# Performance work log

Measured on AMD Instinct MI355X. Metric: run time of the kernel, lower is better.

Reference implementation:

```python
import jax, jax.numpy as jnp
import numpy as np

D_MODEL = 1024
D_INNER = 2048      # expand=2
D_STATE = 128
NHEADS = 32
HEADDIM = 64
DCONV = 4
CONV_DIM = D_INNER + 2 * D_STATE                 # x, B, C channels through conv
D_IN_PROJ = 2 * D_INNER + 2 * D_STATE + NHEADS   # z, xBC, dt
NBLOCKS = 4


def _mlp(x, w1, b1, w2, b2):
    # MLP(2, in, out): Linear(in,in) -> ReLU -> Linear(in,out)
    return jax.nn.relu(x @ w1 + b1) @ w2 + b2


def _mamba2_block(u, Wi, cw, cb, dtb, Alog, Dsk, nw, Wo):
    B, L, _ = u.shape
    zxbcdt = u @ Wi                                        # [B,L,D_IN_PROJ]
    z, xBC, dt = jnp.split(zxbcdt, [D_INNER, D_INNER + CONV_DIM], axis=-1)
    # causal depthwise conv1d, kernel 4
    pad = jnp.pad(xBC, ((0, 0), (DCONV - 1, 0), (0, 0)))
    conv = cb
    for k in range(DCONV):
        conv = conv + pad[:, k:k + L, :] * cw[:, k]
    xBC = jax.nn.silu(conv)
    xh, Bm, Cm = jnp.split(xBC, [D_INNER, D_INNER + D_STATE], axis=-1)
    dt = jax.nn.softplus(dt + dtb)                         # [B,L,H]
    A = -jnp.exp(Alog)                                     # [H], negative
    xh = xh.reshape(B, L, NHEADS, HEADDIM)

    def step(h, inp):
        x_t, dt_t, b_t, c_t = inp                          # [B,H,P],[B,H],[B,N],[B,N]
        dA = jnp.exp(dt_t * A)                             # [B,H]
        h = h * dA[..., None, None] + (dt_t[..., None] * x_t)[..., None] * b_t[:, None, None, :]
        y = jnp.einsum('bhpn,bn->bhp', h, c_t)
        return h, y

    h0 = jnp.zeros((B, NHEADS, HEADDIM, D_STATE), u.dtype)
    _, ys = jax.lax.scan(step, h0, (xh.transpose(1, 0, 2, 3), dt.transpose(1, 0, 2),
                                    Bm.transpose(1, 0, 2), Cm.transpose(1, 0, 2)))
    y = ys.transpose(1, 0, 2, 3) + Dsk[None, None, :, None] * xh   # D skip per head
    y = y.reshape(B, L, D_INNER)
    y = y * jax.nn.silu(z)                                 # gated RMSNorm (gate before norm)
    y = y * jax.lax.rsqrt(jnp.mean(y * y, axis=-1, keepdims=True) + 1e-5) * nw
    return y @ Wo


def setup_inputs() -> dict:
    key = jax.random.key(0)
    ks = jax.random.split(key, 16)
    B, S, STATE = 4, 512, 510
    s = 0.02
    return {
        'x': jax.random.normal(ks[0], (B, S, STATE), jnp.float32),
        'steps_left': jax.random.uniform(ks[1], (B, S, 1), jnp.float32) * 100.0,
        'current_r': jax.random.normal(ks[2], (B, S, 1), jnp.float32),
        'mlp_in_w1': jax.random.normal(ks[3], (STATE + 2, STATE + 2), jnp.float32) * s,
        'mlp_in_b1': jnp.zeros((STATE + 2,), jnp.float32),
        'mlp_in_w2': jax.random.normal(ks[4], (STATE + 2, D_MODEL), jnp.float32) * s,
        'mlp_in_b2': jnp.zeros((D_MODEL,), jnp.float32),
        'W_in': jax.random.normal(ks[5], (NBLOCKS, D_MODEL, D_IN_PROJ), jnp.float32) * s,
        'conv_w': jax.random.normal(ks[6], (NBLOCKS, CONV_DIM, DCONV), jnp.float32) * 0.2,
        'conv_b': jnp.zeros((NBLOCKS, CONV_DIM), jnp.float32),
        'dt_bias': jax.random.normal(ks[7], (NBLOCKS, NHEADS), jnp.float32) * 0.1,
        'A_log': jnp.log(jax.random.uniform(ks[8], (NBLOCKS, NHEADS), jnp.float32, 1.0, 16.0)),
        'D_skip': jnp.ones((NBLOCKS, NHEADS), jnp.float32),
        'norm_w': jnp.ones((NBLOCKS, D_INNER), jnp.float32),
        'W_out': jax.random.normal(ks[9], (NBLOCKS, D_INNER, D_MODEL), jnp.float32) * s,
        'mlp_out_w1': jax.random.normal(ks[10], (D_MODEL, D_MODEL), jnp.float32) * s,
        'mlp_out_b1': jnp.zeros((D_MODEL,), jnp.float32),
        'mlp_out_w2': jax.random.normal(ks[11], (D_MODEL, 1), jnp.float32) * s,
        'mlp_out_b2': jnp.zeros((1,), jnp.float32),
    }


def reference(x, steps_left, current_r,
              mlp_in_w1, mlp_in_b1, mlp_in_w2, mlp_in_b2,
              W_in, conv_w, conv_b, dt_bias, A_log, D_skip, norm_w, W_out,
              mlp_out_w1, mlp_out_b1, mlp_out_w2, mlp_out_b2):
    h = jnp.concatenate([x, steps_left, current_r], axis=-1)   # [B,S,state+2]
    h = _mlp(h, mlp_in_w1, mlp_in_b1, mlp_in_w2, mlp_in_b2)
    for i in range(NBLOCKS):
        h = _mamba2_block(h, W_in[i], conv_w[i], conv_b[i], dt_bias[i],
                          A_log[i], D_skip[i], norm_w[i], W_out[i])
    return _mlp(h, mlp_out_w1, mlp_out_b1, mlp_out_w2, mlp_out_b2)  # [B,S,1]
```

## Files before the change

### kernel.cpp

```cpp
#include <hip/hip_runtime.h>
#include <hip/hip_bf16.h>
#include <math.h>

#define D_MODEL   1024
#define D_INNER   2048
#define D_STATE   128
#define NHEADS    32
#define HEADDIM   64
#define DCONV     4
#define CONV_DIM  (D_INNER + 2 * D_STATE)
#define D_IN_PROJ (2 * D_INNER + 2 * D_STATE + NHEADS)
#define NBLOCKS   4
#define BATCH     4
#define SEQ       512
#define NTOK      (BATCH * SEQ)
#define STATE_IN  510
#define NPAD_IN   4480
#define NSEG      8
#define SEGLEN    64
#define NBH       (BATCH * NHEADS)
#define OFF_B     D_INNER
#define OFF_C     (D_INNER + D_STATE)
#define OFF_DT    (D_IN_PROJ - NHEADS)

typedef _Float16 half8_t __attribute__((ext_vector_type(8)));
typedef float f32x4_t  __attribute__((ext_vector_type(4)));
typedef unsigned short us;

__device__ __forceinline__ us f2h(float f) {
    _Float16 h = (_Float16)f;
    return __builtin_bit_cast(us, h);
}
__device__ __forceinline__ float h2f(us u) {
    return (float)__builtin_bit_cast(_Float16, u);
}
__device__ __forceinline__ void gl2lds16(const us* gp, us* lp) {
    __builtin_amdgcn_global_load_lds(
        (const __attribute__((address_space(1))) unsigned int*)(gp),
        (__attribute__((address_space(3))) unsigned int*)(lp), 16, 0, 0);
}

__global__ void concat_kernel(const float* __restrict__ x,
                              const float* __restrict__ steps,
                              const float* __restrict__ curr,
                              us* __restrict__ hcat)
{
    int idx = blockIdx.x * 256 + threadIdx.x;
    if (idx >= NTOK * 512) return;
    int bl = idx >> 9;
    int c  = idx & 511;
    float v;
    if (c < STATE_IN)       v = x[(size_t)bl * STATE_IN + c];
    else if (c == STATE_IN) v = steps[bl];
    else                    v = curr[bl];
    hcat[idx] = f2h(v);
}

#define NT_TRANS 27904
__global__ __launch_bounds__(256)
void transpose_all_kernel(const float* __restrict__ mi_w1, const float* __restrict__ mi_w2,
                          const float* __restrict__ W_in, const float* __restrict__ W_out,
                          const float* __restrict__ mo_w1,
                          us* __restrict__ wt_mi1, us* __restrict__ wt_mi2,
                          us* __restrict__ wt_in, us* __restrict__ wt_out,
                          us* __restrict__ wt_mo1)
{
    int bid = blockIdx.x;
    const float* W; us* WT; int K, N, ntx, r;
    if (bid < 256)        { W = mi_w1; WT = wt_mi1; K = 512;  N = 512;  ntx = 16;  r = bid; }
    else if (bid < 768)   { W = mi_w2; WT = wt_mi2; K = 512;  N = 1024; ntx = 32;  r = bid - 256; }
    else if (bid < 18688) {
        int rel = bid - 768, i = rel / 4480;
        r = rel - i * 4480;
        W  = W_in  + (size_t)i * D_MODEL * D_IN_PROJ;
        WT = wt_in + (size_t)i * NPAD_IN * 1024;
        K = 1024; N = D_IN_PROJ; ntx = 140;
    }
    else if (bid < 26880) {
        int rel = bid - 18688, i = rel / 2048;
        r = rel - i * 2048;
        W  = W_out  + (size_t)i * D_INNER * D_MODEL;
        WT = wt_out + (size_t)i * 1024 * 2048;
        K = 2048; N = 1024; ntx = 32;
    }
    else { W = mo_w1; WT = wt_mo1; K = 1024; N = 1024; ntx = 32; r = bid - 26880; }
    int n0 = (r % ntx) * 32, k0 = (r / ntx) * 32;

    __shared__ us tile[32][36];
    int t = threadIdx.x;
    int kl = t >> 3, nl = (t & 7) * 4;
    float4 v = make_float4(0.f, 0.f, 0.f, 0.f);
    if (n0 < N) v = *(const float4*)(W + (size_t)(k0 + kl) * N + n0 + nl);
    tile[nl + 0][kl] = f2h(v.x);
    tile[nl + 1][kl] = f2h(v.y);
    tile[nl + 2][kl] = f2h(v.z);
    tile[nl + 3][kl] = f2h(v.w);
    __syncthreads();
    int nl2 = t >> 3, kl2 = (t & 7) * 4;
    ushort4 o;
    o.x = tile[nl2][kl2 + 0];
    o.y = tile[nl2][kl2 + 1];
    o.z = tile[nl2][kl2 + 2];
    o.w = tile[nl2][kl2 + 3];
    *(ushort4*)(WT + (size_t)(n0 + nl2) * K + k0 + kl2) = o;
}

#define PHASE(TT, CUR, STG)                                                     \
    {                                                                           \
        if ((TT) == NT - 1)                                                     \
            asm volatile("s_waitcnt vmcnt(0)" ::: "memory");                    \
        else if constexpr (BN == 128)                                           \
            asm volatile("s_waitcnt vmcnt(4)" ::: "memory");                    \
        else                                                                    \
            asm volatile("s_waitcnt vmcnt(3)" ::: "memory");                    \
        __builtin_amdgcn_s_barrier();                                           \
        if ((TT) + 2 < NT) stage(STG, ((TT) + 2) << 5);                         \
        half8_t af[TI], bfr[4];                                                 \
        _Pragma("unroll")                                                       \
        for (int ti = 0; ti < TI; ++ti) {                                       \
            int rr = wr + ti * 16 + l16;                                        \
            af[ti] = *(const half8_t*)&Al[CUR][rr * 32 + ((g ^ ((rr >> 2) & 3)) * 8)]; \
        }                                                                       \
        _Pragma("unroll")                                                       \
        for (int tj = 0; tj < 4; ++tj) {                                        \
            int rr = wc + tj * 16 + l16;                                        \
            bfr[tj] = *(const half8_t*)&Bl[CUR][rr * 32 + ((g ^ ((rr >> 2) & 3)) * 8)]; \
        }                                                                       \
        _Pragma("unroll")                                                       \
        for (int ti = 0; ti < TI; ++ti)                                         \
            _Pragma("unroll")                                                   \
            for (int tj = 0; tj < 4; ++tj)                                      \
                acc[ti][tj] = __builtin_amdgcn_mfma_f32_16x16x32_f16(           \
                    af[ti], bfr[tj], acc[ti][tj], 0, 0, 0);                     \
    }

template<int BN, int TI>
__global__ __launch_bounds__(256)
void mfma_gemm_f16(const us* __restrict__ A, const us* __restrict__ BT,
                   const float* __restrict__ bias, us* __restrict__ C,
                   int N, int K, int relu)
{
    __shared__ __attribute__((aligned(16))) us Al[3][128 * 32];
    __shared__ __attribute__((aligned(16))) us Bl[3][BN * 32];
    const int tid = threadIdx.x, lane = tid & 63, wave = tid >> 6;
    const int g = lane >> 4, l16 = lane & 15;
    const int wr = (BN == 128) ? (wave >> 1) * 64 : wave * 32;
    const int wc = (BN == 128) ? (wave & 1) * 64 : 0;
    const int m0 = blockIdx.y * 128, n0 = blockIdx.x * BN;
    const int lrow = lane >> 2;
    const int lcol = ((lane & 3) ^ ((lrow >> 2) & 3)) * 8;

    f32x4_t acc[TI][4];
    const f32x4_t zero = {0.f, 0.f, 0.f, 0.f};
#pragma unroll
    for (int i = 0; i < TI; ++i)
#pragma unroll
        for (int j = 0; j < 4; ++j) acc[i][j] = zero;

    const us* abase = A  + (size_t)m0 * K;
    const us* bbase = BT + (size_t)n0 * K;

    auto stage = [&](int buf, int k0) {
#pragma unroll
        for (int s = 0; s < 2; ++s) {
            int rb = wave * 32 + s * 16;
            gl2lds16(abase + (size_t)(rb + lrow) * K + k0 + lcol, &Al[buf][rb * 32]);
        }
#pragma unroll
        for (int s = 0; s < BN / 64; ++s) {
            int rb = wave * (BN / 4) + s * 16;
            gl2lds16(bbase + (size_t)(rb + lrow) * K + k0 + lcol, &Bl[buf][rb * 32]);
        }
    };

    const int NT = K >> 5;
    stage(0, 0);
    stage(1, 32);

    for (int t = 0; t < NT; t += 3) {
        PHASE(t, 0, 2)
        if (t + 1 < NT) PHASE(t + 1, 1, 0)
        if (t + 2 < NT) PHASE(t + 2, 2, 1)
    }

#pragma unroll
    for (int tj = 0; tj < 4; ++tj) {
        int col = n0 + wc + tj * 16 + l16;
        if (col >= N) continue;
        float bv = bias ? bias[col] : 0.f;
#pragma unroll
        for (int ti = 0; ti < TI; ++ti) {
            int rbase = m0 + wr + ti * 16 + g * 4;
#pragma unroll
            for (int r = 0; r < 4; ++r) {
                float v = acc[ti][tj][r] + bv;
                if (relu) v = fmaxf(v, 0.f);
                C[(size_t)(rbase + r) * N + col] = f2h(v);
            }
        }
    }
}

__global__ __launch_bounds__(256)
void conv_silu_kernel(const us* __restrict__ zxbcdt,
                      const float* __restrict__ cw,
                      const float* __restrict__ cb,
                      us* __restrict__ xBCc)
{
    int idx = blockIdx.x * 256 + threadIdx.x;
    if (idx >= NTOK * (CONV_DIM / 4)) return;
    int cq = idx % (CONV_DIM / 4);
    int bl = idx / (CONV_DIM / 4);
    int b  = bl >> 9;
    int l  = bl & 511;
    int c  = cq * 4;
    float4 w0 = *(const float4*)&cw[(c + 0) * DCONV];
    float4 w1 = *(const float4*)&cw[(c + 1) * DCONV];
    float4 w2 = *(const float4*)&cw[(c + 2) * DCONV];
    float4 w3 = *(const float4*)&cw[(c + 3) * DCONV];
    float4 bb = *(const float4*)&cb[c];
    float a0 = bb.x, a1 = bb.y, a2 = bb.z, a3 = bb.w;
    const us* base = zxbcdt + (size_t)(b * SEQ) * D_IN_PROJ + D_INNER + c;
#pragma unroll
    for (int k = 0; k < DCONV; ++k) {
        int ll = l + k - (DCONV - 1);
        if (ll >= 0) {
            ushort4 u = *(const ushort4*)(base + (size_t)ll * D_IN_PROJ);
            a0 = fmaf(h2f(u.x), ((const float*)&w0)[k], a0);
            a1 = fmaf(h2f(u.y), ((const float*)&w1)[k], a1);
            a2 = fmaf(h2f(u.z), ((const float*)&w2)[k], a2);
            a3 = fmaf(h2f(u.w), ((const float*)&w3)[k], a3);
        }
    }
    ushort4 o;
    o.x = f2h(a0 / (1.f + __expf(-a0)));
    o.y = f2h(a1 / (1.f + __expf(-a1)));
    o.z = f2h(a2 / (1.f + __expf(-a2)));
    o.w = f2h(a3 / (1.f + __expf(-a3)));
    *(ushort4*)(xBCc + (size_t)bl * CONV_DIM + c) = o;
}

__global__ __launch_bounds__(256)
void scan_seg_mfma_kernel(const us* __restrict__ zx, const us* __restrict__ xc,
                          const float* __restrict__ dt_bias,
                          const float* __restrict__ A_log,
                          const float* __restrict__ D_skip,
                          float* __restrict__ y, float* __restrict__ alpha,
                          us* __restrict__ Hseg)
{
    __shared__ __attribute__((aligned(16))) us Csh[64 * 128];
    __shared__ __attribute__((aligned(16))) us Bsh[64 * 128];
    __shared__ __attribute__((aligned(16))) us Bt[128 * 64];
    __shared__ __attribute__((aligned(16))) us Xt[64 * 64];
    __shared__ float dt_s[64], ls[64], csc[64];
    us* Ssh = Csh;
    const int bi = blockIdx.x, bh = bi >> 3, seg = bi & 7;
    const int b = bh >> 5, h = bh & 31;
    const int tid = threadIdx.x, lane = tid & 63, w = tid >> 6;
    const int g = lane >> 4, l16 = lane & 15;
    const int t0g = seg * SEGLEN;
    const size_t rowbase = (size_t)(b * SEQ + t0g);

    {
        int rr = lane >> 4, s = lane & 15;
#pragma unroll
        for (int it = 0; it < 4; ++it) {
            int rb = w * 16 + it * 4;
            int row = rb + rr;
            const us* src = xc + (rowbase + row) * CONV_DIM;
            int sw = (s ^ (row & 7)) * 8;
            gl2lds16(src + OFF_C + sw, &Csh[rb * 128]);
            gl2lds16(src + OFF_B + sw, &Bsh[rb * 128]);
        }
    }
#pragma unroll
    for (int qi = 0; qi < 4; ++qi) {
        int idx = tid + qi * 256;
        int pq = idx & 15, j = idx >> 4;
        ushort4 v = *(const ushort4*)(xc + (rowbase + j) * CONV_DIM + h * 64 + pq * 4);
#pragma unroll
        for (int e = 0; e < 4; ++e) {
            int p = pq * 4 + e;
            int pc = ((((j >> 3) ^ (p & 7)) << 3) | (j & 7));
            Xt[p * 64 + pc] = ((const us*)&v)[e];
        }
    }
#pragma unroll
    for (int qi = 0; qi < 8; ++qi) {
        int idx = tid + qi * 256;
        int nq = idx & 31, j = idx >> 5;
        ushort4 v = *(const ushort4*)(xc + (rowbase + j) * CONV_DIM + OFF_B + nq * 4);
#pragma unroll
        for (int e = 0; e < 4; ++e) {
            int n = nq * 4 + e;
            int pc = ((((j >> 3) ^ (n & 7)) << 3) | (j & 7));
            Bt[n * 64 + pc] = ((const us*)&v)[e];
        }
    }
    if (tid < 64) {
        int j = tid;
        float dtraw = h2f(zx[(rowbase + j) * D_IN_PROJ + OFF_DT + h]) + dt_bias[h];
        float dtv = (dtraw > 20.f) ? dtraw : log1pf(expf(dtraw));
        float ld = dtv * (-expf(A_log[h]));
#pragma unroll
        for (int o = 1; o < 64; o <<= 1) {
            float v = __shfl_up(ld, o);
            if (j >= o) ld += v;
        }
        float al = expf(ld);
        dt_s[j] = dtv;
        ls[j] = ld;
        alpha[(size_t)bh * SEQ + t0g + j] = al;
        float cend = __shfl(ld, 63);
        csc[j] = dtv * expf(cend - ld);
    }
    __syncthreads();

    const float Dsk = D_skip[h];
    const f32x4_t vzero = {0.f, 0.f, 0.f, 0.f};

    f32x4_t acc1[4];
#pragma unroll
    for (int jt = 0; jt < 4; ++jt) acc1[jt] = vzero;
    {
        int ia = w * 16 + l16;
#pragma unroll
        for (int ks = 0; ks < 4; ++ks) {
            half8_t a = *(const half8_t*)&Csh[ia * 128 + (((ks * 4 + g) ^ (ia & 7)) << 3)];
#pragma unroll
            for (int jt = 0; jt < 4; ++jt) {
                int jr = jt * 16 + l16;
                half8_t bfr = *(const half8_t*)&Bsh[jr * 128 + (((ks * 4 + g) ^ (jr & 7)) << 3)];
                acc1[jt] = __builtin_amdgcn_mfma_f32_16x16x32_f16(a, bfr, acc1[jt], 0, 0, 0);
            }
        }
    }
    __syncthreads();

    {
        int i0 = w * 16 + g * 4;
        float lsi[4];
#pragma unroll
        for (int r = 0; r < 4; ++r) lsi[r] = ls[i0 + r];
#pragma unroll
        for (int jt = 0; jt < 4; ++jt) {
            int j = jt * 16 + l16;
            float lj = ls[j], dj = dt_s[j];
#pragma unroll
            for (int r = 0; r < 4; ++r) {
                int i = i0 + r;
                float v = 0.f;
                if (j < i)       v = acc1[jt][r] * dj * __expf(lsi[r] - lj);
                else if (j == i) v = acc1[jt][r] * dj + Dsk;
                int pc = ((((j >> 3) ^ (i & 7)) << 3) | (j & 7));
                Ssh[i * 64 + pc] = f2h(v);
            }
        }
    }
    __syncthreads();

    f32x4_t acc2[4];
#pragma unroll
    for (int nt = 0; nt < 4; ++nt) acc2[nt] = vzero;
    {
        int ia = w * 16 + l16;
#pragma unroll
        for (int ks = 0; ks < 2; ++ks) {
            half8_t a = *(const half8_t*)&Ssh[ia * 64 + (((ks * 4 + g) ^ (ia & 7)) << 3)];
#pragma unroll
            for (int nt = 0; nt < 4; ++nt) {
                int pr = nt * 16 + l16;
                half8_t bfr = *(const half8_t*)&Xt[pr * 64 + (((ks * 4 + g) ^ (pr & 7)) << 3)];
                acc2[nt] = __builtin_amdgcn_mfma_f32_16x16x32_f16(a, bfr, acc2[nt], 0, 0, 0);
            }
        }
    }
    {
        int i0 = w * 16 + g * 4;
#pragma unroll
        for (int nt = 0; nt < 4; ++nt) {
            int p = nt * 16 + l16;
#pragma unroll
            for (int r = 0; r < 4; ++r)
                y[(rowbase + i0 + r) * D_INNER + h * 64 + p] = acc2[nt][r];
        }
    }
    f32x4_t acc3[8];
#pragma unroll
    for (int nt = 0; nt < 8; ++nt) acc3[nt] = vzero;
    {
        int pa = w * 16 + l16;
#pragma unroll
        for (int ks = 0; ks < 2; ++ks) {
            half8_t araw = *(const half8_t*)&Xt[pa * 64 + (((ks * 4 + g) ^ (pa & 7)) << 3)];
            half8_t a;
#pragma unroll
            for (int e = 0; e < 8; ++e)
                a[e] = (_Float16)((float)araw[e] * csc[ks * 32 + g * 8 + e]);
#pragma unroll
            for (int nt = 0; nt < 8; ++nt) {
                int nr = nt * 16 + l16;
                half8_t bfr = *(const half8_t*)&Bt[nr * 64 + (((ks * 4 + g) ^ (nr & 7)) << 3)];
                acc3[nt] = __builtin_amdgcn_mfma_f32_16x16x32_f16(a, bfr, acc3[nt], 0, 0, 0);
            }
        }
    }
    {
        int p0 = w * 16 + g * 4;
#pragma unroll
        for (int nt = 0; nt < 8; ++nt) {
            int n = nt * 16 + l16;
#pragma unroll
            for (int r = 0; r < 4; ++r)
                Hseg[((size_t)bi * 64 + p0 + r) * 128 + n] = f2h(acc3[nt][r]);
        }
    }
}

__global__ __launch_bounds__(512)
void state_fixup_kernel(const float* __restrict__ alpha, us* __restrict__ Hseg)
{
    const int bh = blockIdx.x;
    const int t = threadIdx.x, p = t >> 3, ng = t & 7;
    float carry[16];
#pragma unroll
    for (int j = 0; j < 16; ++j) carry[j] = 0.f;
    for (int seg = 0; seg < NSEG; ++seg) {
        us* hs = Hseg + (((size_t)bh * NSEG + seg) * 64 + p) * 128;
        float ae = alpha[(size_t)bh * SEQ + seg * SEGLEN + SEGLEN - 1];
        float tmp[16];
#pragma unroll
        for (int q = 0; q < 4; ++q) {
            ushort4 u = *(const ushort4*)(hs + ng * 4 + q * 32);
            tmp[q*4+0] = h2f(u.x); tmp[q*4+1] = h2f(u.y);
            tmp[q*4+2] = h2f(u.z); tmp[q*4+3] = h2f(u.w);
        }
#pragma unroll
        for (int q = 0; q < 4; ++q) {
            ushort4 o;
            o.x = f2h(carry[q*4+0]); o.y = f2h(carry[q*4+1]);
            o.z = f2h(carry[q*4+2]); o.w = f2h(carry[q*4+3]);
            *(ushort4*)(hs + ng * 4 + q * 32) = o;
        }
#pragma unroll
        for (int j = 0; j < 16; ++j) carry[j] = fmaf(carry[j], ae, tmp[j]);
    }
}

__global__ __launch_bounds__(256)
void correct_mfma_kernel(const us* __restrict__ xc, const float* __restrict__ alpha,
                         const us* __restrict__ Hseg, float* __restrict__ y)
{
    __shared__ __attribute__((aligned(16))) us Csh[64 * 128];
    __shared__ __attribute__((aligned(16))) us Hsh[64 * 128];
    __shared__ float als_s[64];
    const int bi = blockIdx.x;
    const int bh = bi / 7, seg = 1 + (bi % 7);
    const int b = bh >> 5, h = bh & 31;
    const int tid = threadIdx.x, lane = tid & 63, w = tid >> 6;
    const int g = lane >> 4, l16 = lane & 15;
    const int t0g = seg * SEGLEN;
    const size_t rowbase = (size_t)(b * SEQ + t0g);
    const size_t hbase = (size_t)(bh * NSEG + seg) * 64;

    {
        int rr = lane >> 4, s = lane & 15;
#pragma unroll
        for (int it = 0; it < 4; ++it) {
            int rb = w * 16 + it * 4;
            int row = rb + rr;
            int sw = (s ^ (row & 7)) * 8;
            gl2lds16(xc + (rowbase + row) * CONV_DIM + OFF_C + sw, &Csh[rb * 128]);
            gl2lds16(Hseg + (hbase + row) * 128 + sw, &Hsh[rb * 128]);
        }
    }
    if (tid < 64) als_s[tid] = alpha[(size_t)bh * SEQ + t0g + tid];
    __syncthreads();

    const f32x4_t vzero = {0.f, 0.f, 0.f, 0.f};
    f32x4_t acc[4];
#pragma unroll
    for (int nt = 0; nt < 4; ++nt) acc[nt] = vzero;
    int ia = w * 16 + l16;
#pragma unroll
    for (int ks = 0; ks < 4; ++ks) {
        half8_t a = *(const half8_t*)&Csh[ia * 128 + (((ks * 4 + g) ^ (ia & 7)) << 3)];
#pragma unroll
        for (int nt = 0; nt < 4; ++nt) {
            int pr = nt * 16 + l16;
            half8_t bfr = *(const half8_t*)&Hsh[pr * 128 + (((ks * 4 + g) ^ (pr & 7)) << 3)];
            acc[nt] = __builtin_amdgcn_mfma_f32_16x16x32_f16(a, bfr, acc[nt], 0, 0, 0);
        }
    }
    int i0 = w * 16 + g * 4;
#pragma unroll
    for (int nt = 0; nt < 4; ++nt) {
        int p = nt * 16 + l16;
#pragma unroll
        for (int r = 0; r < 4; ++r) {
            size_t idx = (rowbase + i0 + r) * D_INNER + h * 64 + p;
            y[idx] += als_s[i0 + r] * acc[nt][r];
        }
    }
}

__global__ __launch_bounds__(256)
void gated_rmsnorm_kernel(const float* __restrict__ y,
                          const us* __restrict__ zxbcdt,
                          const float* __restrict__ norm_w,
                          us* __restrict__ yn)
{
    int bl = blockIdx.x;
    int t  = threadIdx.x;
    const float* yr = y + (size_t)bl * D_INNER;
    const us* zr = zxbcdt + (size_t)bl * D_IN_PROJ;
    us* outr = yn + (size_t)bl * D_INNER;

    float gv[8];
    float ss = 0.f;
#pragma unroll
    for (int q = 0; q < 8; ++q) {
        int j = t + q * 256;
        float z = h2f(zr[j]);
        float g = yr[j] * (z / (1.f + __expf(-z)));
        gv[q] = g;
        ss += g * g;
    }
    __shared__ float red[256];
    red[t] = ss;
    __syncthreads();
    for (int w = 128; w > 0; w >>= 1) {
        if (t < w) red[t] += red[t + w];
        __syncthreads();
    }
    float rs = rsqrtf(red[0] / (float)D_INNER + 1e-5f);
#pragma unroll
    for (int q = 0; q < 8; ++q) {
        int j = t + q * 256;
        outr[j] = f2h(gv[q] * rs * norm_w[j]);
    }
}

__global__ __launch_bounds__(256)
void final_dot_kernel(const us* __restrict__ t1,
                      const float* __restrict__ w2,
                      const float* __restrict__ b2,
                      float* __restrict__ out)
{
    int bl = blockIdx.x;
    int t  = threadIdx.x;
    float s = 0.f;
    for (int j = t; j < D_MODEL; j += 256)
        s = fmaf(h2f(t1[(size_t)bl * D_MODEL + j]), w2[j], s);
    __shared__ float red[256];
    red[t] = s;
    __syncthreads();
    for (int w = 128; w > 0; w >>= 1) {
        if (t < w) red[t] += red[t + w];
        __syncthreads();
    }
    if (t == 0) out[bl] = red[0] + b2[0];
}

extern "C" void kernel_launch(void* const* d_in, const int* in_sizes, int n_in,
                              void* d_out, int out_size, void* d_ws, size_t ws_size,
                              hipStream_t stream)
{
    const float* x        = (const float*)d_in[0];
    const float* steps    = (const float*)d_in[1];
    const float* curr     = (const float*)d_in[2];
    const float* mi_w1    = (const float*)d_in[3];
    const float* mi_b1    = (const float*)d_in[4];
    const float* mi_w2    = (const float*)d_in[5];
    const float* mi_b2    = (const float*)d_in[6];
    const float* W_in     = (const float*)d_in[7];
    const float* conv_w   = (const float*)d_in[8];
    const float* conv_b   = (const float*)d_in[9];
    const float* dt_bias  = (const float*)d_in[10];
    const float* A_log    = (const float*)d_in[11];
    const float* D_skip   = (const float*)d_in[12];
    const float* norm_w   = (const float*)d_in[13];
    const float* W_out    = (const float*)d_in[14];
    const float* mo_w1    = (const float*)d_in[15];
    const float* mo_b1    = (const float*)d_in[16];
    const float* mo_w2    = (const float*)d_in[17];
    const float* mo_b2    = (const float*)d_in[18];
    float* out = (float*)d_out;

    us* wt_mi1 = (us*)d_ws;
    us* wt_mi2 = wt_mi1 + (size_t)512 * 512;
    us* wt_in  = wt_mi2 + (size_t)1024 * 512;
    us* wt_out = wt_in  + (size_t)4 * NPAD_IN * 1024;
    us* wt_mo1 = wt_out + (size_t)4 * 1024 * 2048;
    us* Hseg   = wt_mo1 + (size_t)1024 * 1024;
    us* hcat   = Hseg   + (size_t)NBH * NSEG * 64 * 128;
    us* h      = hcat   + (size_t)NTOK * 512;
    us* zxb    = h      + (size_t)NTOK * D_MODEL;
    us* xc     = zxb    + (size_t)NTOK * D_IN_PROJ;
    us* yn     = xc     + (size_t)NTOK * CONV_DIM;
    us* t0     = zxb;
    us* t1     = xc;
    float* fbase = (float*)((((uintptr_t)(yn + (size_t)NTOK * D_INNER)) + 255)
                            & ~(uintptr_t)255);
    float* y     = fbase;
    float* alpha = y + (size_t)NTOK * D_INNER;

    transpose_all_kernel<<<NT_TRANS, 256, 0, stream>>>(
        mi_w1, mi_w2, W_in, W_out, mo_w1,
        wt_mi1, wt_mi2, wt_in, wt_out, wt_mo1);

    concat_kernel<<<(NTOK * 512 + 255) / 256, 256, 0, stream>>>(x, steps, curr, hcat);

    mfma_gemm_f16<64, 2><<<dim3(512/64, NTOK/128), 256, 0, stream>>>(
        hcat, wt_mi1, mi_b1, t0, 512, 512, 1);
    mfma_gemm_f16<64, 2><<<dim3(1024/64, NTOK/128), 256, 0, stream>>>(
        t0, wt_mi2, mi_b2, h, 1024, 512, 0);

    for (int i = 0; i < NBLOCKS; ++i) {
        mfma_gemm_f16<128, 4><<<dim3(NPAD_IN/128, NTOK/128), 256, 0, stream>>>(
            h, wt_in + (size_t)i * NPAD_IN * 1024, nullptr, zxb, D_IN_PROJ, D_MODEL, 0);
        conv_silu_kernel<<<(NTOK * (CONV_DIM/4) + 255) / 256, 256, 0, stream>>>(
            zxb, conv_w + (size_t)i * CONV_DIM * DCONV, conv_b + (size_t)i * CONV_DIM, xc);
        scan_seg_mfma_kernel<<<NBH * NSEG, 256, 0, stream>>>(
            zxb, xc, dt_bias + i * NHEADS, A_log + i * NHEADS, D_skip + i * NHEADS,
            y, alpha, Hseg);
        state_fixup_kernel<<<NBH, 512, 0, stream>>>(alpha, Hseg);
        correct_mfma_kernel<<<NBH * (NSEG - 1), 256, 0, stream>>>(xc, alpha, Hseg, y);
        gated_rmsnorm_kernel<<<NTOK, 256, 0, stream>>>(
            y, zxb, norm_w + (size_t)i * D_INNER, yn);
        mfma_gemm_f16<64, 2><<<dim3(1024/64, NTOK/128), 256, 0, stream>>>(
            yn, wt_out + (size_t)i * 1024 * 2048, nullptr, h, 1024, 2048, 0);
    }

    mfma_gemm_f16<64, 2><<<dim3(1024/64, NTOK/128), 256, 0, stream>>>(
        h, wt_mo1, mo_b1, t1, 1024, 1024, 1);
    final_dot_kernel<<<NTOK, 256, 0, stream>>>(t1, mo_w2, mo_b2, out);
}
```

Before: 747.9 us.

## Use larger weight-transpose tiles, smaller MLP-in GEMM tiles, and split state fixup

The weight transpose kernel now handles 64x64 fp32 tiles per block instead of 32x32. It stores fp32 in a padded LDS tile and writes 8-wide fp16 vectors, so far fewer blocks are launched. The GEMM template gains a BM parameter, and the two small input-MLP GEMMs now use 64x64 tiles to put more blocks on the device. The state fixup kernel splits each head's state across two blocks to double its parallelism. The trade-offs are more LDS per transpose block and lower per-block reuse in the small GEMMs.

```diff
diff --git a/kernel.cpp b/kernel.cpp
--- a/kernel.cpp
+++ b/kernel.cpp
@@ -26,6 +26,7 @@
 typedef _Float16 half8_t __attribute__((ext_vector_type(8)));
 typedef float f32x4_t  __attribute__((ext_vector_type(4)));
 typedef unsigned short us;
+typedef unsigned short us8 __attribute__((ext_vector_type(8)));
 
 __device__ __forceinline__ us f2h(float f) {
     _Float16 h = (_Float16)f;
@@ -56,7 +57,7 @@
     hcat[idx] = f2h(v);
 }
 
-#define NT_TRANS 27904
+#define NT_TRANS 6976
 __global__ __launch_bounds__(256)
 void transpose_all_kernel(const float* __restrict__ mi_w1, const float* __restrict__ mi_w2,
                           const float* __restrict__ W_in, const float* __restrict__ W_out,
@@ -67,52 +68,60 @@
 {
     int bid = blockIdx.x;
     const float* W; us* WT; int K, N, ntx, r;
-    if (bid < 256)        { W = mi_w1; WT = wt_mi1; K = 512;  N = 512;  ntx = 16;  r = bid; }
-    else if (bid < 768)   { W = mi_w2; WT = wt_mi2; K = 512;  N = 1024; ntx = 32;  r = bid - 256; }
-    else if (bid < 18688) {
-        int rel = bid - 768, i = rel / 4480;
-        r = rel - i * 4480;
+    if (bid < 64)        { W = mi_w1; WT = wt_mi1; K = 512;  N = 512;  ntx = 8;  r = bid; }
+    else if (bid < 192)  { W = mi_w2; WT = wt_mi2; K = 512;  N = 1024; ntx = 16; r = bid - 64; }
+    else if (bid < 4672) {
+        int rel = bid - 192, i = rel / 1120;
+        r = rel - i * 1120;
         W  = W_in  + (size_t)i * D_MODEL * D_IN_PROJ;
         WT = wt_in + (size_t)i * NPAD_IN * 1024;
-        K = 1024; N = D_IN_PROJ; ntx = 140;
-    }
-    else if (bid < 26880) {
-        int rel = bid - 18688, i = rel / 2048;
-        r = rel - i * 2048;
+        K = 1024; N = D_IN_PROJ; ntx = 70;
+    }
+    else if (bid < 6720) {
+        int rel = bid - 4672, i = rel / 512;
+        r = rel - i * 512;
         W  = W_out  + (size_t)i * D_INNER * D_MODEL;
         WT = wt_out + (size_t)i * 1024 * 2048;
-        K = 2048; N = 1024; ntx = 32;
-    }
-    else { W = mo_w1; WT = wt_mo1; K = 1024; N = 1024; ntx = 32; r = bid - 26880; }
-    int n0 = (r % ntx) * 32, k0 = (r / ntx) * 32;
-
-    __shared__ us tile[32][36];
+        K = 2048; N = 1024; ntx = 16;
+    }
+    else { W = mo_w1; WT = wt_mo1; K = 1024; N = 1024; ntx = 16; r = bid - 6720; }
+    int n0 = (r % ntx) * 64, k0 = (r / ntx) * 64;
+
+    __shared__ float tile[64][65];
     int t = threadIdx.x;
-    int kl = t >> 3, nl = (t & 7) * 4;
-    float4 v = make_float4(0.f, 0.f, 0.f, 0.f);
-    if (n0 < N) v = *(const float4*)(W + (size_t)(k0 + kl) * N + n0 + nl);
-    tile[nl + 0][kl] = f2h(v.x);
-    tile[nl + 1][kl] = f2h(v.y);
-    tile[nl + 2][kl] = f2h(v.z);
-    tile[nl + 3][kl] = f2h(v.w);
+    int kl = t >> 4;
+    int nl = (t & 15) * 4;
+#pragma unroll
+    for (int it = 0; it < 4; ++it) {
+        int k = kl + it * 16;
+        float4 v = make_float4(0.f, 0.f, 0.f, 0.f);
+        if (n0 + nl < N) v = *(const float4*)(W + (size_t)(k0 + k) * N + n0 + nl);
+        tile[k][nl + 0] = v.x; tile[k][nl + 1] = v.y;
+        tile[k][nl + 2] = v.z; tile[k][nl + 3] = v.w;
+    }
     __syncthreads();
-    int nl2 = t >> 3, kl2 = (t & 7) * 4;
-    ushort4 o;
-    o.x = tile[nl2][kl2 + 0];
-    o.y = tile[nl2][kl2 + 1];
-    o.z = tile[nl2][kl2 + 2];
-    o.w = tile[nl2][kl2 + 3];
-    *(ushort4*)(WT + (size_t)(n0 + nl2) * K + k0 + kl2) = o;
+    int a  = t & 7;
+    int nr = t >> 3;
+#pragma unroll
+    for (int s = 0; s < 2; ++s) {
+        int n = nr + s * 32;
+        us8 o;
+#pragma unroll
+        for (int j = 0; j < 8; ++j) o[j] = f2h(tile[a * 8 + j][n]);
+        *(us8*)(WT + (size_t)(n0 + n) * K + k0 + a * 8) = o;
+    }
 }
 
 #define PHASE(TT, CUR, STG)                                                     \
     {                                                                           \
         if ((TT) == NT - 1)                                                     \
             asm volatile("s_waitcnt vmcnt(0)" ::: "memory");                    \
-        else if constexpr (BN == 128)                                           \
+        else if constexpr (BM / 64 + BN / 64 == 4)                              \
             asm volatile("s_waitcnt vmcnt(4)" ::: "memory");                    \
+        else if constexpr (BM / 64 + BN / 64 == 3)                              \
+            asm volatile("s_waitcnt vmcnt(3)" ::: "memory");                    \
         else                                                                    \
-            asm volatile("s_waitcnt vmcnt(3)" ::: "memory");                    \
+            asm volatile("s_waitcnt vmcnt(2)" ::: "memory");                    \
         __builtin_amdgcn_s_barrier();                                           \
         if ((TT) + 2 < NT) stage(STG, ((TT) + 2) << 5);                         \
         half8_t af[TI], bfr[4];                                                 \
@@ -134,19 +143,19 @@
                     af[ti], bfr[tj], acc[ti][tj], 0, 0, 0);                     \
     }
 
-template<int BN, int TI>
+template<int BM, int BN, int TI>
 __global__ __launch_bounds__(256)
 void mfma_gemm_f16(const us* __restrict__ A, const us* __restrict__ BT,
                    const float* __restrict__ bias, us* __restrict__ C,
                    int N, int K, int relu)
 {
-    __shared__ __attribute__((aligned(16))) us Al[3][128 * 32];
+    __shared__ __attribute__((aligned(16))) us Al[3][BM * 32];
     __shared__ __attribute__((aligned(16))) us Bl[3][BN * 32];
     const int tid = threadIdx.x, lane = tid & 63, wave = tid >> 6;
     const int g = lane >> 4, l16 = lane & 15;
-    const int wr = (BN == 128) ? (wave >> 1) * 64 : wave * 32;
+    const int wr = (BN == 128) ? (wave >> 1) * 64 : wave * (BM / 4);
     const int wc = (BN == 128) ? (wave & 1) * 64 : 0;
-    const int m0 = blockIdx.y * 128, n0 = blockIdx.x * BN;
+    const int m0 = blockIdx.y * BM, n0 = blockIdx.x * BN;
     const int lrow = lane >> 2;
     const int lcol = ((lane & 3) ^ ((lrow >> 2) & 3)) * 8;
 
@@ -162,8 +171,8 @@
 
     auto stage = [&](int buf, int k0) {
 #pragma unroll
-        for (int s = 0; s < 2; ++s) {
-            int rb = wave * 32 + s * 16;
+        for (int s = 0; s < BM / 64; ++s) {
+            int rb = wave * (BM / 4) + s * 16;
             gl2lds16(abase + (size_t)(rb + lrow) * K + k0 + lcol, &Al[buf][rb * 32]);
         }
 #pragma unroll
@@ -420,30 +429,31 @@
 __global__ __launch_bounds__(512)
 void state_fixup_kernel(const float* __restrict__ alpha, us* __restrict__ Hseg)
 {
-    const int bh = blockIdx.x;
+    const int bh = blockIdx.x >> 1, hf = blockIdx.x & 1;
     const int t = threadIdx.x, p = t >> 3, ng = t & 7;
-    float carry[16];
-#pragma unroll
-    for (int j = 0; j < 16; ++j) carry[j] = 0.f;
+    const int off = hf * 64 + ng * 8;
+    float carry[8];
+#pragma unroll
+    for (int j = 0; j < 8; ++j) carry[j] = 0.f;
     for (int seg = 0; seg < NSEG; ++seg) {
-        us* hs = Hseg + (((size_t)bh * NSEG + seg) * 64 + p) * 128;
+        us* hs = Hseg + (((size_t)bh * NSEG + seg) * 64 + p) * 128 + off;
         float ae = alpha[(size_t)bh * SEQ + seg * SEGLEN + SEGLEN - 1];
-        float tmp[16];
-#pragma unroll
-        for (int q = 0; q < 4; ++q) {
-            ushort4 u = *(const ushort4*)(hs + ng * 4 + q * 32);
+        float tmp[8];
+#pragma unroll
+        for (int q = 0; q < 2; ++q) {
+            ushort4 u = *(const ushort4*)(hs + q * 4);
             tmp[q*4+0] = h2f(u.x); tmp[q*4+1] = h2f(u.y);
             tmp[q*4+2] = h2f(u.z); tmp[q*4+3] = h2f(u.w);
         }
 #pragma unroll
-        for (int q = 0; q < 4; ++q) {
+        for (int q = 0; q < 2; ++q) {
             ushort4 o;
             o.x = f2h(carry[q*4+0]); o.y = f2h(carry[q*4+1]);
             o.z = f2h(carry[q*4+2]); o.w = f2h(carry[q*4+3]);
-            *(ushort4*)(hs + ng * 4 + q * 32) = o;
-        }
-#pragma unroll
-        for (int j = 0; j < 16; ++j) carry[j] = fmaf(carry[j], ae, tmp[j]);
+            *(ushort4*)(hs + q * 4) = o;
+        }
+#pragma unroll
+        for (int j = 0; j < 8; ++j) carry[j] = fmaf(carry[j], ae, tmp[j]);
     }
 }
 
@@ -611,28 +621,28 @@
 
     concat_kernel<<<(NTOK * 512 + 255) / 256, 256, 0, stream>>>(x, steps, curr, hcat);
 
-    mfma_gemm_f16<64, 2><<<dim3(512/64, NTOK/128), 256, 0, stream>>>(
+    mfma_gemm_f16<64, 64, 1><<<dim3(512/64, NTOK/64), 256, 0, stream>>>(
         hcat, wt_mi1, mi_b1, t0, 512, 512, 1);
-    mfma_gemm_f16<64, 2><<<dim3(1024/64, NTOK/128), 256, 0, stream>>>(
+    mfma_gemm_f16<64, 64, 1><<<dim3(1024/64, NTOK/64), 256, 0, stream>>>(
         t0, wt_mi2, mi_b2, h, 1024, 512, 0);
 
     for (int i = 0; i < NBLOCKS; ++i) {
-        mfma_gemm_f16<128, 4><<<dim3(NPAD_IN/128, NTOK/128), 256, 0, stream>>>(
+        mfma_gemm_f16<128, 128, 4><<<dim3(NPAD_IN/128, NTOK/128), 256, 0, stream>>>(
             h, wt_in + (size_t)i * NPAD_IN * 1024, nullptr, zxb, D_IN_PROJ, D_MODEL, 0);
         conv_silu_kernel<<<(NTOK * (CONV_DIM/4) + 255) / 256, 256, 0, stream>>>(
             zxb, conv_w + (size_t)i * CONV_DIM * DCONV, conv_b + (size_t)i * CONV_DIM, xc);
         scan_seg_mfma_kernel<<<NBH * NSEG, 256, 0, stream>>>(
             zxb, xc, dt_bias + i * NHEADS, A_log + i * NHEADS, D_skip + i * NHEADS,
             y, alpha, Hseg);
-        state_fixup_kernel<<<NBH, 512, 0, stream>>>(alpha, Hseg);
+        state_fixup_kernel<<<NBH * 2, 512, 0, stream>>>(alpha, Hseg);
         correct_mfma_kernel<<<NBH * (NSEG - 1), 256, 0, stream>>>(xc, alpha, Hseg, y);
         gated_rmsnorm_kernel<<<NTOK, 256, 0, stream>>>(
             y, zxb, norm_w + (size_t)i * D_INNER, yn);
-        mfma_gemm_f16<64, 2><<<dim3(1024/64, NTOK/128), 256, 0, stream>>>(
+        mfma_gemm_f16<128, 64, 2><<<dim3(1024/64, NTOK/128), 256, 0, stream>>>(
             yn, wt_out + (size_t)i * 1024 * 2048, nullptr, h, 1024, 2048, 0);
     }
 
-    mfma_gemm_f16<64, 2><<<dim3(1024/64, NTOK/128), 256, 0, stream>>>(
+    mfma_gemm_f16<128, 64, 2><<<dim3(1024/64, NTOK/128), 256, 0, stream>>>(
         h, wt_mo1, mo_b1, t1, 1024, 1024, 1);
     final_dot_kernel<<<NTOK, 256, 0, stream>>>(t1, mo_w2, mo_b2, out);
 }
```

Measured after the change: 734.2 us. About the same (-1.8%).
